# Kernel tuning notes

Measured on AMD Instinct MI355X. Metric: run time of the kernel, lower is better.

## Reference

```python
import jax, jax.numpy as jnp
import numpy as np
from jax import lax

DIM = 48
HEADS = 8
B, H, W = 4, 256, 256
EPS = 1e-12  # torch F.normalize eps


def conv1x1(x, w):
    # x: [b,c,h,w], w: [out,c] (1x1 conv, no bias)
    return jnp.einsum('bchw,oc->bohw', x, w)


def dwconv3x3(x, w):
    # depthwise 3x3, padding 1; w: [C,1,3,3]
    return lax.conv_general_dilated(
        x, w, window_strides=(1, 1), padding=((1, 1), (1, 1)),
        dimension_numbers=('NCHW', 'OIHW', 'NCHW'),
        feature_group_count=x.shape[1])


def setup_inputs() -> dict:
    key = jax.random.key(0)
    ks = jax.random.split(key, 8)
    s = 0.05
    return {
        'fea_0': jax.random.normal(ks[0], (B, DIM, H, W), jnp.float32),
        'fea_1': jax.random.normal(ks[1], (B, DIM, H, W), jnp.float32),
        'qk_w': jax.random.normal(ks[2], (2 * DIM, DIM), jnp.float32) * s,
        'qk_dw_w': jax.random.normal(ks[3], (2 * DIM, 1, 3, 3), jnp.float32) * s,
        'v_w': jax.random.normal(ks[4], (DIM, DIM), jnp.float32) * s,
        'v_dw_w': jax.random.normal(ks[5], (DIM, 1, 3, 3), jnp.float32) * s,
        'proj_w': jax.random.normal(ks[6], (DIM, DIM), jnp.float32) * s,
        'temperature': jnp.ones((HEADS, 1, 1), jnp.float32),
    }


def reference(fea_0, fea_1, qk_w, qk_dw_w, v_w, v_dw_w, proj_w, temperature):
    b, c, h, w = fea_0.shape
    ch = c // HEADS  # channels per head
    qk = dwconv3x3(conv1x1(fea_0, qk_w), qk_dw_w)
    q, k = jnp.split(qk, 2, axis=1)
    v = dwconv3x3(conv1x1(fea_1, v_w), v_dw_w)
    # [b, head, c_per_head, h*w]
    q = q.reshape(b, HEADS, ch, h * w)
    k = k.reshape(b, HEADS, ch, h * w)
    v = v.reshape(b, HEADS, ch, h * w)
    q = q / jnp.maximum(jnp.linalg.norm(q, axis=-1, keepdims=True), EPS)
    k = k / jnp.maximum(jnp.linalg.norm(k, axis=-1, keepdims=True), EPS)
    attn = jnp.einsum('bhcn,bhdn->bhcd', q, k) * temperature[None]
    attn = jax.nn.softmax(attn, axis=-1)
    out = jnp.einsum('bhcd,bhdn->bhcn', attn, v)
    out = out.reshape(b, c, h, w)
    return conv1x1(out, proj_w)
```

## Files before the change

kernel.cpp:

```cpp
#include <hip/hip_runtime.h>
#include <cstddef>

#define IMG 256
#define HW 65536
#define NB 4
#define NC_IN 48
#define NHEADS 8
#define OHALO 18
#define OHP (OHALO*OHALO)

typedef short bf16x8 __attribute__((ext_vector_type(8)));
typedef float f32x4 __attribute__((ext_vector_type(4)));
typedef float f32x16 __attribute__((ext_vector_type(16)));

__device__ __forceinline__ unsigned short f2bf(float f) {
    unsigned int x = __float_as_uint(f);
    unsigned int r = (x + 0x7fffu + ((x >> 16) & 1u)) >> 16;
    return (unsigned short)r;
}

__device__ __forceinline__ int xcd_map(int bid, int nwg) {
    const int q = nwg >> 3, r = nwg & 7;
    const int x = bid & 7, i = bid >> 3;
    return (x < r ? x * (q + 1) : r * (q + 1) + (x - r) * q) + i;
}

__global__ __launch_bounds__(256) void prep_qcw_kernel(
    const float* __restrict__ qk_w, const float* __restrict__ qk_dw,
    unsigned short* __restrict__ qcwb) {
    const int idx = blockIdx.x * 256 + threadIdx.x;
    if (idx >= 9 * 128 * 48) return;
    const int e = idx % 48;
    const int s = (idx / 48) & 127;
    const int tap = idx / (48 * 128);
    const int head = s >> 4, sub = s & 15;
    float v = 0.f;
    if (sub < 12) {
        const int row = (sub < 6) ? (head * 6 + sub) : (48 + head * 6 + (sub - 6));
        v = qk_dw[row * 9 + tap] * qk_w[row * 48 + e];
    }
    qcwb[idx] = f2bf(v);
}

__global__ __launch_bounds__(256, 3) void fused_qk_stats_kernel(
    const float* __restrict__ fea0, const unsigned short* __restrict__ qcwb,
    float* __restrict__ stats) {
    __shared__ __align__(16) unsigned short xs[OHP][56];
    __shared__ __align__(16) unsigned short sg[4][16][72];
    __shared__ float sacc[384];

    const int tid = threadIdx.x;
    const int b = blockIdx.y;
    const int tile = xcd_map(blockIdx.x, 256);
    const int tx = tile & 15, ty = tile >> 4;
    const float* fb = fea0 + (size_t)b * NC_IN * HW;

    for (int i = tid; i < 384; i += 256) sacc[i] = 0.f;

    for (int hp = tid; hp < OHP; hp += 256) {
        const int hx = hp % OHALO, hy = hp / OHALO;
        const int gx = tx * 16 + hx - 1, gy = ty * 16 + hy - 1;
        const bool inb = ((unsigned)gx < (unsigned)IMG) && ((unsigned)gy < (unsigned)IMG);
        const int pix = inb ? (gy * IMG + gx) : 0;
#pragma unroll
        for (int j = 0; j < 6; ++j) {
            bf16x8 t;
#pragma unroll
            for (int c = 0; c < 8; ++c) {
                const float v = inb ? fb[(size_t)(j * 8 + c) * HW + pix] : 0.f;
                t[c] = (short)f2bf(v);
            }
            *(bf16x8*)&xs[hp][j * 8] = t;
        }
    }
    __syncthreads();

    const int wave = tid >> 6, lane = tid & 63;
    const int l31 = lane & 31, lhi = lane >> 5;
    const int opx0 = wave * 64 + l31, opx1 = opx0 + 32;
    const int r0 = (opx0 >> 4) * OHALO + (opx0 & 15);
    const int r1 = (opx1 >> 4) * OHALO + (opx1 & 15);
    const int fr = lane & 15, fg = lane >> 4;

#define DO_STATS(CA, CB, hbase)                                                   \
    {                                                                             \
        _Pragma("unroll")                                                         \
        for (int hh = 0; hh < 2; ++hh) {                                          \
            _Pragma("unroll")                                                     \
            for (int rq = 0; rq < 2; ++rq) {                                      \
                if (!(rq && lhi)) {                                               \
                    _Pragma("unroll")                                             \
                    for (int j = 0; j < 4; ++j) {                                 \
                        const int sub = j + 8 * rq + 4 * lhi;                     \
                        sg[wave][sub][l31] = f2bf(CA[hh * 8 + rq * 4 + j]);       \
                        sg[wave][sub][32 + l31] = f2bf(CB[hh * 8 + rq * 4 + j]);  \
                    }                                                             \
                }                                                                 \
            }                                                                     \
            asm volatile("s_waitcnt lgkmcnt(0)" ::: "memory");                    \
            __builtin_amdgcn_sched_barrier(0);                                    \
            const bf16x8 a0 = *(const bf16x8*)&sg[wave][fr][fg * 8];              \
            const bf16x8 a1 = *(const bf16x8*)&sg[wave][fr][32 + fg * 8];         \
            asm volatile("s_waitcnt lgkmcnt(0)" ::: "memory");                    \
            __builtin_amdgcn_sched_barrier(0);                                    \
            f32x4 c4 = {0.f, 0.f, 0.f, 0.f};                                      \
            c4 = __builtin_amdgcn_mfma_f32_16x16x32_bf16(a0, a0, c4, 0, 0, 0);    \
            c4 = __builtin_amdgcn_mfma_f32_16x16x32_bf16(a1, a1, c4, 0, 0, 0);    \
            const int h = (hbase) + hh;                                           \
            _Pragma("unroll")                                                     \
            for (int r = 0; r < 4; ++r) {                                         \
                const int crow = fg * 4 + r;                                      \
                const float vv = c4[r];                                           \
                if (crow < 6) {                                                   \
                    if (fr == crow) atomicAdd(&sacc[h * 6 + crow], vv);           \
                    else if (fr >= 6 && fr < 12)                                  \
                        atomicAdd(&sacc[96 + h * 36 + crow * 6 + (fr - 6)], vv);  \
                } else if (crow < 12 && fr == crow) {                             \
                    atomicAdd(&sacc[48 + h * 6 + (crow - 6)], vv);                \
                }                                                                 \
            }                                                                     \
        }                                                                         \
    }

#pragma unroll
    for (int p = 0; p < 2; ++p) {
        f32x16 C00, C01, C10, C11;
#pragma unroll
        for (int r = 0; r < 16; ++r) { C00[r] = 0.f; C01[r] = 0.f; C10[r] = 0.f; C11[r] = 0.f; }

#pragma unroll
        for (int t9 = 0; t9 < 9; ++t9) {
            const int hoff = (t9 / 3) * OHALO + (t9 % 3);
#pragma unroll
            for (int ks = 0; ks < 3; ++ks) {
                const int kb = ks * 16 + lhi * 8;
                const bf16x8 b0 = *(const bf16x8*)&xs[r0 + hoff][kb];
                const bf16x8 b1 = *(const bf16x8*)&xs[r1 + hoff][kb];
                const bf16x8 a0 = *(const bf16x8*)&qcwb[((size_t)t9 * 128 + p * 64 + l31) * 48 + kb];
                const bf16x8 a1 = *(const bf16x8*)&qcwb[((size_t)t9 * 128 + p * 64 + 32 + l31) * 48 + kb];
                C00 = __builtin_amdgcn_mfma_f32_32x32x16_bf16(a0, b0, C00, 0, 0, 0);
                C01 = __builtin_amdgcn_mfma_f32_32x32x16_bf16(a0, b1, C01, 0, 0, 0);
                C10 = __builtin_amdgcn_mfma_f32_32x32x16_bf16(a1, b0, C10, 0, 0, 0);
                C11 = __builtin_amdgcn_mfma_f32_32x32x16_bf16(a1, b1, C11, 0, 0, 0);
            }
        }

        DO_STATS(C00, C01, p * 4 + 0)
        DO_STATS(C10, C11, p * 4 + 2)
    }
#undef DO_STATS

    __syncthreads();
    for (int i = tid; i < 384; i += 256) atomicAdd(&stats[b * 384 + i], sacc[i]);
}

__global__ __launch_bounds__(256) void softmax_w2_cw_kernel(
    const float* __restrict__ stats, const float* __restrict__ proj_w,
    const float* __restrict__ temperature, const float* __restrict__ v_w,
    const float* __restrict__ v_dw, unsigned short* __restrict__ cwb) {
    const int b = blockIdx.x;
    const int tid = threadIdx.x;
    __shared__ float attn[NHEADS * 36];
    __shared__ float W2s[48 * 48];
    const float* sb = stats + b * 384;

    if (tid < 48) {
        const int h = tid / 6, cc = tid % 6;
        float nq = fmaxf(sqrtf(sb[tid]), 1e-12f);
        const float tmp = temperature[h];
        float lo[6];
#pragma unroll
        for (int d = 0; d < 6; ++d) {
            const float nk = fmaxf(sqrtf(sb[48 + h * 6 + d]), 1e-12f);
            lo[d] = sb[96 + h * 36 + cc * 6 + d] / (nq * nk) * tmp;
        }
        float m = lo[0];
#pragma unroll
        for (int d = 1; d < 6; ++d) m = fmaxf(m, lo[d]);
        float s = 0.f;
#pragma unroll
        for (int d = 0; d < 6; ++d) { lo[d] = expf(lo[d] - m); s += lo[d]; }
        const float inv = 1.f / s;
#pragma unroll
        for (int d = 0; d < 6; ++d) attn[h * 36 + cc * 6 + d] = lo[d] * inv;
    }
    __syncthreads();

    for (int idx = tid; idx < 48 * 48; idx += 256) {
        const int c = idx / 48, dg = idx % 48;
        const int h = dg / 6, hd = dg % 6;
        float s = 0.f;
#pragma unroll
        for (int cc = 0; cc < 6; ++cc)
            s = fmaf(proj_w[c * 48 + h * 6 + cc], attn[h * 36 + cc * 6 + hd], s);
        W2s[idx] = s;
    }
    __syncthreads();

    for (int p = 0; p < 9; ++p) {
        const int pair = p * 256 + tid;
        const int c = pair / 48, e = pair % 48;
        float acc[9];
#pragma unroll
        for (int t = 0; t < 9; ++t) acc[t] = 0.f;
        for (int d = 0; d < 48; ++d) {
            const float wv = W2s[c * 48 + d] * v_w[d * 48 + e];
#pragma unroll
            for (int t = 0; t < 9; ++t)
                acc[t] = fmaf(wv, v_dw[d * 9 + t], acc[t]);
        }
#pragma unroll
        for (int t = 0; t < 9; ++t)
            cwb[(size_t)b * 20736 + (size_t)(t * 48 + c) * 48 + e] = f2bf(acc[t]);
    }
}

__global__ __launch_bounds__(256) void conv3x3_out_kernel(
    const float* __restrict__ fea1, const unsigned short* __restrict__ cwb,
    float* __restrict__ out) {
    __shared__ __align__(16) unsigned short xs[OHP][56];

    const int tid = threadIdx.x;
    const int b = blockIdx.y;
    const int tile = xcd_map(blockIdx.x, 256);
    const int tx = tile & 15, ty = tile >> 4;
    const float* fb = fea1 + (size_t)b * NC_IN * HW;

    for (int hp = tid; hp < OHP; hp += 256) {
        const int hx = hp % OHALO, hy = hp / OHALO;
        const int gx = tx * 16 + hx - 1, gy = ty * 16 + hy - 1;
        const bool inb = ((unsigned)gx < (unsigned)IMG) && ((unsigned)gy < (unsigned)IMG);
        const int pix = inb ? (gy * IMG + gx) : 0;
#pragma unroll
        for (int j = 0; j < 6; ++j) {
            bf16x8 t;
#pragma unroll
            for (int c = 0; c < 8; ++c) {
                const float v = inb ? fb[(size_t)(j * 8 + c) * HW + pix] : 0.f;
                t[c] = (short)f2bf(v);
            }
            *(bf16x8*)&xs[hp][j * 8] = t;
        }
    }
    __syncthreads();

    const int wave = tid >> 6, lane = tid & 63;
    const int l31 = lane & 31, lhi = lane >> 5;
    const int opx0 = wave * 64 + l31, opx1 = opx0 + 32;
    const int r0 = (opx0 >> 4) * OHALO + (opx0 & 15);
    const int r1 = (opx1 >> 4) * OHALO + (opx1 & 15);
    const unsigned short* cb = cwb + (size_t)b * 20736;
    const bool m1ok = l31 < 16;

    f32x16 C00, C01, C10, C11;
#pragma unroll
    for (int r = 0; r < 16; ++r) { C00[r] = 0.f; C01[r] = 0.f; C10[r] = 0.f; C11[r] = 0.f; }

#pragma unroll
    for (int dy = 0; dy < 3; ++dy)
#pragma unroll
        for (int dx = 0; dx < 3; ++dx) {
            const int t9 = dy * 3 + dx;
            const int hoff = dy * OHALO + dx;
#pragma unroll
            for (int ks = 0; ks < 3; ++ks) {
                const int kb = ks * 16 + lhi * 8;
                const bf16x8 a0 = *(const bf16x8*)&cb[(size_t)(t9 * 48 + l31) * 48 + kb];
                bf16x8 a1;
#pragma unroll
                for (int j = 0; j < 8; ++j) a1[j] = 0;
                if (m1ok) a1 = *(const bf16x8*)&cb[(size_t)(t9 * 48 + 32 + l31) * 48 + kb];
                const bf16x8 b0 = *(const bf16x8*)&xs[r0 + hoff][kb];
                const bf16x8 b1 = *(const bf16x8*)&xs[r1 + hoff][kb];
                C00 = __builtin_amdgcn_mfma_f32_32x32x16_bf16(a0, b0, C00, 0, 0, 0);
                C01 = __builtin_amdgcn_mfma_f32_32x32x16_bf16(a0, b1, C01, 0, 0, 0);
                C10 = __builtin_amdgcn_mfma_f32_32x32x16_bf16(a1, b0, C10, 0, 0, 0);
                C11 = __builtin_amdgcn_mfma_f32_32x32x16_bf16(a1, b1, C11, 0, 0, 0);
            }
        }

    float* ob = out + (size_t)b * NC_IN * HW;
    const int g0 = (ty * 16 + (opx0 >> 4)) * IMG + tx * 16 + (opx0 & 15);
    const int g1 = (ty * 16 + (opx1 >> 4)) * IMG + tx * 16 + (opx1 & 15);
#pragma unroll
    for (int r = 0; r < 16; ++r) {
        const int row = (r & 3) + 8 * (r >> 2) + 4 * lhi;
        ob[(size_t)row * HW + g0] = C00[r];
        ob[(size_t)row * HW + g1] = C01[r];
        const int row1 = 32 + row;
        if (row1 < 48) {
            ob[(size_t)row1 * HW + g0] = C10[r];
            ob[(size_t)row1 * HW + g1] = C11[r];
        }
    }
}

extern "C" void kernel_launch(void* const* d_in, const int* in_sizes, int n_in,
                              void* d_out, int out_size, void* d_ws, size_t ws_size,
                              hipStream_t stream) {
    const float* fea0 = (const float*)d_in[0];
    const float* fea1 = (const float*)d_in[1];
    const float* qk_w = (const float*)d_in[2];
    const float* qk_dw = (const float*)d_in[3];
    const float* v_w = (const float*)d_in[4];
    const float* v_dw = (const float*)d_in[5];
    const float* proj_w = (const float*)d_in[6];
    const float* temperature = (const float*)d_in[7];
    float* out = (float*)d_out;

    char* ws = (char*)d_ws;
    float* stats = (float*)ws;
    unsigned short* cwb = (unsigned short*)(ws + 8192);
    unsigned short* qcwb = (unsigned short*)(ws + 8192 + 165888);

    hipMemsetAsync(stats, 0, (size_t)NB * 384 * sizeof(float), stream);

    prep_qcw_kernel<<<216, 256, 0, stream>>>(qk_w, qk_dw, qcwb);
    fused_qk_stats_kernel<<<dim3(256, NB), 256, 0, stream>>>(fea0, qcwb, stats);
    softmax_w2_cw_kernel<<<NB, 256, 0, stream>>>(stats, proj_w, temperature, v_w, v_dw, cwb);
    conv3x3_out_kernel<<<dim3(256, NB), 256, 0, stream>>>(fea1, cwb, out);
}
```

Measured before the change: 129.5 us.

## Use 32x16 tiles with 512 threads and K-chunked halo staging in both convs

Both the QK-stats and output conv kernels move from 16x16 tiles with 256 threads to 32x16 tiles with 512 threads. Input channels are staged through LDS in three 16-channel chunks, so the LDS buffer shrinks and each wave can reuse one weight fragment across four pixel rows. Weight buffers are relaid out as [tap][kchunk][row][16] with zero-padded rows to match. This lowers halo overhead and per-MFMA weight loads, at the cost of extra barriers per chunk, more accumulator registers, and non-coalesced channel-strided global loads done three times per tile.

Result: faster. 121.9 us (-5.8%).

```diff
diff --git a/kernel.cpp b/kernel.cpp
--- a/kernel.cpp
+++ b/kernel.cpp
@@ -4,10 +4,14 @@
 #define IMG 256
 #define HW 65536
 #define NB 4
-#define NC_IN 48
 #define NHEADS 8
-#define OHALO 18
-#define OHP (OHALO*OHALO)
+#define TW 32
+#define TH 16
+#define HAW 34
+#define HAH 18
+#define HP2 (HAW*HAH)
+#define NTILE 128
+#define XSP 24
 
 typedef short bf16x8 __attribute__((ext_vector_type(8)));
 typedef float f32x4 __attribute__((ext_vector_type(4)));
@@ -29,57 +33,80 @@
     const float* __restrict__ qk_w, const float* __restrict__ qk_dw,
     unsigned short* __restrict__ qcwb) {
     const int idx = blockIdx.x * 256 + threadIdx.x;
-    if (idx >= 9 * 128 * 48) return;
-    const int e = idx % 48;
-    const int s = (idx / 48) & 127;
-    const int tap = idx / (48 * 128);
-    const int head = s >> 4, sub = s & 15;
+    const int e16 = idx & 15;
+    const int slot = (idx >> 4) & 127;
+    const int tk = idx >> 11;
+    const int ks = tk % 3;
+    const int head = slot >> 4, sub = slot & 15;
     float v = 0.f;
     if (sub < 12) {
         const int row = (sub < 6) ? (head * 6 + sub) : (48 + head * 6 + (sub - 6));
-        v = qk_dw[row * 9 + tap] * qk_w[row * 48 + e];
+        v = qk_dw[row * 9 + tk / 3] * qk_w[row * 48 + ks * 16 + e16];
     }
     qcwb[idx] = f2bf(v);
 }
 
-__global__ __launch_bounds__(256, 3) void fused_qk_stats_kernel(
+__global__ __launch_bounds__(512, 2) void fused_qk_stats_kernel(
     const float* __restrict__ fea0, const unsigned short* __restrict__ qcwb,
     float* __restrict__ stats) {
-    __shared__ __align__(16) unsigned short xs[OHP][56];
-    __shared__ __align__(16) unsigned short sg[4][16][72];
+    __shared__ __align__(16) unsigned short xs[HP2][XSP];
+    __shared__ __align__(16) unsigned short sg[8][16][72];
     __shared__ float sacc[384];
 
     const int tid = threadIdx.x;
     const int b = blockIdx.y;
-    const int tile = xcd_map(blockIdx.x, 256);
-    const int tx = tile & 15, ty = tile >> 4;
-    const float* fb = fea0 + (size_t)b * NC_IN * HW;
-
-    for (int i = tid; i < 384; i += 256) sacc[i] = 0.f;
-
-    for (int hp = tid; hp < OHP; hp += 256) {
-        const int hx = hp % OHALO, hy = hp / OHALO;
-        const int gx = tx * 16 + hx - 1, gy = ty * 16 + hy - 1;
-        const bool inb = ((unsigned)gx < (unsigned)IMG) && ((unsigned)gy < (unsigned)IMG);
-        const int pix = inb ? (gy * IMG + gx) : 0;
-#pragma unroll
-        for (int j = 0; j < 6; ++j) {
-            bf16x8 t;
-#pragma unroll
-            for (int c = 0; c < 8; ++c) {
-                const float v = inb ? fb[(size_t)(j * 8 + c) * HW + pix] : 0.f;
-                t[c] = (short)f2bf(v);
-            }
-            *(bf16x8*)&xs[hp][j * 8] = t;
-        }
-    }
-    __syncthreads();
+    const int tile = xcd_map(blockIdx.x, NTILE);
+    const int tx = tile & 7, ty = tile >> 3;
+    const float* fb = fea0 + (size_t)b * 48 * HW;
+
+    for (int i = tid; i < 384; i += 512) sacc[i] = 0.f;
 
     const int wave = tid >> 6, lane = tid & 63;
     const int l31 = lane & 31, lhi = lane >> 5;
-    const int opx0 = wave * 64 + l31, opx1 = opx0 + 32;
-    const int r0 = (opx0 >> 4) * OHALO + (opx0 & 15);
-    const int r1 = (opx1 >> 4) * OHALO + (opx1 & 15);
+    const int p = wave >> 2, g = wave & 3;
+
+    f32x16 C[2][4];
+#pragma unroll
+    for (int m = 0; m < 2; ++m)
+#pragma unroll
+        for (int nf = 0; nf < 4; ++nf)
+#pragma unroll
+            for (int r = 0; r < 16; ++r) C[m][nf][r] = 0.f;
+
+#pragma unroll
+    for (int ks = 0; ks < 3; ++ks) {
+        __syncthreads();
+        for (int hp = tid; hp < HP2; hp += 512) {
+            const int hx = hp % HAW, hy = hp / HAW;
+            const int gx = tx * TW + hx - 1, gy = ty * TH + hy - 1;
+            const bool inb = ((unsigned)gx < (unsigned)IMG) && ((unsigned)gy < (unsigned)IMG);
+            const int pix = inb ? (gy * IMG + gx) : 0;
+            bf16x8 t0, t1;
+#pragma unroll
+            for (int c = 0; c < 8; ++c) {
+                t0[c] = (short)f2bf(inb ? fb[(size_t)(ks * 16 + c) * HW + pix] : 0.f);
+                t1[c] = (short)f2bf(inb ? fb[(size_t)(ks * 16 + 8 + c) * HW + pix] : 0.f);
+            }
+            *(bf16x8*)&xs[hp][0] = t0;
+            *(bf16x8*)&xs[hp][8] = t1;
+        }
+        __syncthreads();
+
+#pragma unroll
+        for (int tap = 0; tap < 9; ++tap) {
+            const int dy = tap / 3, dx = tap % 3;
+            const bf16x8 a0 = *(const bf16x8*)&qcwb[(size_t)((tap * 3 + ks) * 128 + p * 64 + l31) * 16 + lhi * 8];
+            const bf16x8 a1 = *(const bf16x8*)&qcwb[(size_t)((tap * 3 + ks) * 128 + p * 64 + 32 + l31) * 16 + lhi * 8];
+#pragma unroll
+            for (int nf = 0; nf < 4; ++nf) {
+                const int hrow = (4 * g + nf + dy) * HAW + l31 + dx;
+                const bf16x8 bb = *(const bf16x8*)&xs[hrow][lhi * 8];
+                C[0][nf] = __builtin_amdgcn_mfma_f32_32x32x16_bf16(a0, bb, C[0][nf], 0, 0, 0);
+                C[1][nf] = __builtin_amdgcn_mfma_f32_32x32x16_bf16(a1, bb, C[1][nf], 0, 0, 0);
+            }
+        }
+    }
+
     const int fr = lane & 15, fg = lane >> 4;
 
 #define DO_STATS(CA, CB, hbase)                                                   \
@@ -123,35 +150,14 @@
     }
 
 #pragma unroll
-    for (int p = 0; p < 2; ++p) {
-        f32x16 C00, C01, C10, C11;
-#pragma unroll
-        for (int r = 0; r < 16; ++r) { C00[r] = 0.f; C01[r] = 0.f; C10[r] = 0.f; C11[r] = 0.f; }
-
-#pragma unroll
-        for (int t9 = 0; t9 < 9; ++t9) {
-            const int hoff = (t9 / 3) * OHALO + (t9 % 3);
-#pragma unroll
-            for (int ks = 0; ks < 3; ++ks) {
-                const int kb = ks * 16 + lhi * 8;
-                const bf16x8 b0 = *(const bf16x8*)&xs[r0 + hoff][kb];
-                const bf16x8 b1 = *(const bf16x8*)&xs[r1 + hoff][kb];
-                const bf16x8 a0 = *(const bf16x8*)&qcwb[((size_t)t9 * 128 + p * 64 + l31) * 48 + kb];
-                const bf16x8 a1 = *(const bf16x8*)&qcwb[((size_t)t9 * 128 + p * 64 + 32 + l31) * 48 + kb];
-                C00 = __builtin_amdgcn_mfma_f32_32x32x16_bf16(a0, b0, C00, 0, 0, 0);
-                C01 = __builtin_amdgcn_mfma_f32_32x32x16_bf16(a0, b1, C01, 0, 0, 0);
-                C10 = __builtin_amdgcn_mfma_f32_32x32x16_bf16(a1, b0, C10, 0, 0, 0);
-                C11 = __builtin_amdgcn_mfma_f32_32x32x16_bf16(a1, b1, C11, 0, 0, 0);
-            }
-        }
-
-        DO_STATS(C00, C01, p * 4 + 0)
-        DO_STATS(C10, C11, p * 4 + 2)
+    for (int m = 0; m < 2; ++m) {
+        DO_STATS(C[m][0], C[m][1], p * 4 + m * 2)
+        DO_STATS(C[m][2], C[m][3], p * 4 + m * 2)
     }
 #undef DO_STATS
 
     __syncthreads();
-    for (int i = tid; i < 384; i += 256) atomicAdd(&stats[b * 384 + i], sacc[i]);
+    for (int i = tid; i < 384; i += 512) atomicAdd(&stats[b * 384 + i], sacc[i]);
 }
 
 __global__ __launch_bounds__(256) void softmax_w2_cw_kernel(
@@ -197,8 +203,9 @@
     }
     __syncthreads();
 
-    for (int p = 0; p < 9; ++p) {
-        const int pair = p * 256 + tid;
+    unsigned short* cb = cwb + (size_t)b * 27648;
+    for (int pp = 0; pp < 9; ++pp) {
+        const int pair = pp * 256 + tid;
         const int c = pair / 48, e = pair % 48;
         float acc[9];
 #pragma unroll
@@ -211,86 +218,78 @@
         }
 #pragma unroll
         for (int t = 0; t < 9; ++t)
-            cwb[(size_t)b * 20736 + (size_t)(t * 48 + c) * 48 + e] = f2bf(acc[t]);
-    }
-}
-
-__global__ __launch_bounds__(256) void conv3x3_out_kernel(
+            cb[(size_t)((t * 3 + (e >> 4)) * 64 + c) * 16 + (e & 15)] = f2bf(acc[t]);
+    }
+    for (int i = tid; i < 6912; i += 256) {
+        const int e16 = i & 15;
+        const int cp = 48 + ((i >> 4) & 15);
+        const int tk = i >> 8;
+        cb[(size_t)(tk * 64 + cp) * 16 + e16] = 0;
+    }
+}
+
+__global__ __launch_bounds__(512, 2) void conv3x3_out_kernel(
     const float* __restrict__ fea1, const unsigned short* __restrict__ cwb,
     float* __restrict__ out) {
-    __shared__ __align__(16) unsigned short xs[OHP][56];
+    __shared__ __align__(16) unsigned short xs[HP2][XSP];
 
     const int tid = threadIdx.x;
     const int b = blockIdx.y;
-    const int tile = xcd_map(blockIdx.x, 256);
-    const int tx = tile & 15, ty = tile >> 4;
-    const float* fb = fea1 + (size_t)b * NC_IN * HW;
-
-    for (int hp = tid; hp < OHP; hp += 256) {
-        const int hx = hp % OHALO, hy = hp / OHALO;
-        const int gx = tx * 16 + hx - 1, gy = ty * 16 + hy - 1;
-        const bool inb = ((unsigned)gx < (unsigned)IMG) && ((unsigned)gy < (unsigned)IMG);
-        const int pix = inb ? (gy * IMG + gx) : 0;
-#pragma unroll
-        for (int j = 0; j < 6; ++j) {
-            bf16x8 t;
-#pragma unroll
-            for (int c = 0; c < 8; ++c) {
-                const float v = inb ? fb[(size_t)(j * 8 + c) * HW + pix] : 0.f;
-                t[c] = (short)f2bf(v);
-            }
-            *(bf16x8*)&xs[hp][j * 8] = t;
-        }
-    }
-    __syncthreads();
+    const int tile = xcd_map(blockIdx.x, NTILE);
+    const int tx = tile & 7, ty = tile >> 3;
+    const float* fb = fea1 + (size_t)b * 48 * HW;
+    const unsigned short* cb = cwb + (size_t)b * 27648;
 
     const int wave = tid >> 6, lane = tid & 63;
     const int l31 = lane & 31, lhi = lane >> 5;
-    const int opx0 = wave * 64 + l31, opx1 = opx0 + 32;
-    const int r0 = (opx0 >> 4) * OHALO + (opx0 & 15);
-    const int r1 = (opx1 >> 4) * OHALO + (opx1 & 15);
-    const unsigned short* cb = cwb + (size_t)b * 20736;
-    const bool m1ok = l31 < 16;
-
-    f32x16 C00, C01, C10, C11;
-#pragma unroll
-    for (int r = 0; r < 16; ++r) { C00[r] = 0.f; C01[r] = 0.f; C10[r] = 0.f; C11[r] = 0.f; }
-
-#pragma unroll
-    for (int dy = 0; dy < 3; ++dy)
-#pragma unroll
-        for (int dx = 0; dx < 3; ++dx) {
-            const int t9 = dy * 3 + dx;
-            const int hoff = dy * OHALO + dx;
-#pragma unroll
-            for (int ks = 0; ks < 3; ++ks) {
-                const int kb = ks * 16 + lhi * 8;
-                const bf16x8 a0 = *(const bf16x8*)&cb[(size_t)(t9 * 48 + l31) * 48 + kb];
-                bf16x8 a1;
-#pragma unroll
-                for (int j = 0; j < 8; ++j) a1[j] = 0;
-                if (m1ok) a1 = *(const bf16x8*)&cb[(size_t)(t9 * 48 + 32 + l31) * 48 + kb];
-                const bf16x8 b0 = *(const bf16x8*)&xs[r0 + hoff][kb];
-                const bf16x8 b1 = *(const bf16x8*)&xs[r1 + hoff][kb];
-                C00 = __builtin_amdgcn_mfma_f32_32x32x16_bf16(a0, b0, C00, 0, 0, 0);
-                C01 = __builtin_amdgcn_mfma_f32_32x32x16_bf16(a0, b1, C01, 0, 0, 0);
-                C10 = __builtin_amdgcn_mfma_f32_32x32x16_bf16(a1, b0, C10, 0, 0, 0);
-                C11 = __builtin_amdgcn_mfma_f32_32x32x16_bf16(a1, b1, C11, 0, 0, 0);
+    const int m = wave & 1, g = wave >> 1;
+
+    f32x16 C[4];
+#pragma unroll
+    for (int nf = 0; nf < 4; ++nf)
+#pragma unroll
+        for (int r = 0; r < 16; ++r) C[nf][r] = 0.f;
+
+#pragma unroll
+    for (int ks = 0; ks < 3; ++ks) {
+        __syncthreads();
+        for (int hp = tid; hp < HP2; hp += 512) {
+            const int hx = hp % HAW, hy = hp / HAW;
+            const int gx = tx * TW + hx - 1, gy = ty * TH + hy - 1;
+            const bool inb = ((unsigned)gx < (unsigned)IMG) && ((unsigned)gy < (unsigned)IMG);
+            const int pix = inb ? (gy * IMG + gx) : 0;
+            bf16x8 t0, t1;
+#pragma unroll
+            for (int c = 0; c < 8; ++c) {
+                t0[c] = (short)f2bf(inb ? fb[(size_t)(ks * 16 + c) * HW + pix] : 0.f);
+                t1[c] = (short)f2bf(inb ? fb[(size_t)(ks * 16 + 8 + c) * HW + pix] : 0.f);
             }
-        }
-
-    float* ob = out + (size_t)b * NC_IN * HW;
-    const int g0 = (ty * 16 + (opx0 >> 4)) * IMG + tx * 16 + (opx0 & 15);
-    const int g1 = (ty * 16 + (opx1 >> 4)) * IMG + tx * 16 + (opx1 & 15);
-#pragma unroll
-    for (int r = 0; r < 16; ++r) {
-        const int row = (r & 3) + 8 * (r >> 2) + 4 * lhi;
-        ob[(size_t)row * HW + g0] = C00[r];
-        ob[(size_t)row * HW + g1] = C01[r];
-        const int row1 = 32 + row;
-        if (row1 < 48) {
-            ob[(size_t)row1 * HW + g0] = C10[r];
-            ob[(size_t)row1 * HW + g1] = C11[r];
+            *(bf16x8*)&xs[hp][0] = t0;
+            *(bf16x8*)&xs[hp][8] = t1;
+        }
+        __syncthreads();
+
+#pragma unroll
+        for (int tap = 0; tap < 9; ++tap) {
+            const int dy = tap / 3, dx = tap % 3;
+            const bf16x8 a = *(const bf16x8*)&cb[(size_t)((tap * 3 + ks) * 64 + m * 32 + l31) * 16 + lhi * 8];
+#pragma unroll
+            for (int nf = 0; nf < 4; ++nf) {
+                const int hrow = (4 * g + nf + dy) * HAW + l31 + dx;
+                const bf16x8 bb = *(const bf16x8*)&xs[hrow][lhi * 8];
+                C[nf] = __builtin_amdgcn_mfma_f32_32x32x16_bf16(a, bb, C[nf], 0, 0, 0);
+            }
+        }
+    }
+
+    float* ob = out + (size_t)b * 48 * HW;
+#pragma unroll
+    for (int nf = 0; nf < 4; ++nf) {
+        const int gpx = (ty * TH + 4 * g + nf) * IMG + tx * TW + l31;
+#pragma unroll
+        for (int r = 0; r < 16; ++r) {
+            const int och = m * 32 + (r & 3) + 8 * (r >> 2) + 4 * lhi;
+            if (m == 0 || r < 8) ob[(size_t)och * HW + gpx] = C[nf][r];
         }
     }
 }
@@ -311,12 +310,12 @@
     char* ws = (char*)d_ws;
     float* stats = (float*)ws;
     unsigned short* cwb = (unsigned short*)(ws + 8192);
-    unsigned short* qcwb = (unsigned short*)(ws + 8192 + 165888);
+    unsigned short* qcwb = (unsigned short*)(ws + 8192 + 221184);
 
     hipMemsetAsync(stats, 0, (size_t)NB * 384 * sizeof(float), stream);
 
     prep_qcw_kernel<<<216, 256, 0, stream>>>(qk_w, qk_dw, qcwb);
-    fused_qk_stats_kernel<<<dim3(256, NB), 256, 0, stream>>>(fea0, qcwb, stats);
+    fused_qk_stats_kernel<<<dim3(NTILE, NB), 512, 0, stream>>>(fea0, qcwb, stats);
     softmax_w2_cw_kernel<<<NB, 256, 0, stream>>>(stats, proj_w, temperature, v_w, v_dw, cwb);
-    conv3x3_out_kernel<<<dim3(256, NB), 256, 0, stream>>>(fea1, cwb, out);
-}
+    conv3x3_out_kernel<<<dim3(NTILE, NB), 512, 0, stream>>>(fea1, cwb, out);
+}
```
